# Optimization experiments

Measured on AMD Instinct MI355X. Metric: run time of the kernel, lower is better.

The kernel has to match this reference:

```python
import jax, jax.numpy as jnp
import numpy as np

Y_SCALE = 0.01  # fixed weight quantization scale (q_scale of the int8 weights)


def setup_inputs() -> dict:
    key = jax.random.key(0)
    kx, kw, kb = jax.random.split(key, 3)
    B, S, IN, OUT = 4, 2048, 4096, 4096
    x = jax.random.normal(kx, (B, S, IN), dtype=jnp.float32)
    # int8 quantized weights, stored transposed as (in_features, out_features)
    weight_q = jax.random.randint(kw, (IN, OUT), -128, 128, dtype=jnp.int32)
    bias = jax.random.normal(kb, (OUT,), dtype=jnp.float32)
    return {"x": x, "weight_q": weight_q, "bias": bias}


def reference(x, weight_q, bias):
    # Per-batch-sample dynamic activation scale: max(|x_i|)/128 over each [S, IN] slice
    x_scale = jnp.max(jnp.abs(x), axis=(1, 2), keepdims=True) / 128.0  # [B,1,1]
    # int8 quantize: round + clip
    xq = jnp.clip(jnp.round(x / x_scale), -128, 127).astype(jnp.int8)  # [B,S,IN]
    wq = weight_q.astype(jnp.int8)                                      # [IN,OUT]
    c = jax.lax.dot_general(
        xq, wq,
        dimension_numbers=(((2,), (0,)), ((), ())),
        preferred_element_type=jnp.int32,
    )  # [B,S,OUT]
    # dequantize and bias-add
    y = c.astype(jnp.float32) * (x_scale * Y_SCALE)
    return y + bias
```

## Files before the change

### kernel.cpp

```cpp
#include <hip/hip_runtime.h>
#include <stdint.h>

#define K_DIM 4096
#define N_DIM 4096
#define M_DIM 8192
#define S_ROWS 2048
#define NT 32

typedef int v4i __attribute__((ext_vector_type(4)));

__device__ __forceinline__ void gload16(const void* g, void* l) {
    __builtin_amdgcn_global_load_lds(
        (const __attribute__((address_space(1))) unsigned int*)g,
        (__attribute__((address_space(3))) unsigned int*)l, 16, 0, 0);
}

__device__ __forceinline__ void barrier() {
    asm volatile("" ::: "memory");
    __builtin_amdgcn_s_barrier();
    asm volatile("" ::: "memory");
}

__global__ void prep1_kernel(const float* __restrict__ x, unsigned* __restrict__ amax,
                             const int* __restrict__ wq, char* __restrict__ wt) {
    __shared__ unsigned lds[64 * 17];
    if (blockIdx.x < 4096) {
        int b = blockIdx.x >> 10;
        int bx = blockIdx.x & 1023;
        const float4* xb = (const float4*)(x + (size_t)b * S_ROWS * K_DIM);
        int tid = bx * 256 + threadIdx.x;
        const int stride = 1024 * 256;
        float m = 0.f;
#pragma unroll
        for (int i = 0; i < 8; ++i) {
            float4 v = xb[tid + i * stride];
            m = fmaxf(m, fmaxf(fmaxf(fabsf(v.x), fabsf(v.y)),
                               fmaxf(fabsf(v.z), fabsf(v.w))));
        }
#pragma unroll
        for (int off = 32; off; off >>= 1)
            m = fmaxf(m, __shfl_xor(m, off));
        float* red = (float*)lds;
        if ((threadIdx.x & 63) == 0) red[threadIdx.x >> 6] = m;
        __syncthreads();
        if (threadIdx.x == 0) {
            m = fmaxf(fmaxf(red[0], red[1]), fmaxf(red[2], red[3]));
            atomicMax(&amax[b], __float_as_uint(m));
        }
    } else {
        int wb = blockIdx.x - 4096;
        int n0 = (wb & 63) * 64;
        int k0 = (wb >> 6) * 64;
        int t = threadIdx.x;
        int c = t & 63;
        int g = t >> 6;
#pragma unroll
        for (int rep = 0; rep < 4; ++rep) {
            int kb = g * 16 + rep * 4;
            int v0 = wq[(size_t)(k0 + kb + 0) * N_DIM + n0 + c];
            int v1 = wq[(size_t)(k0 + kb + 1) * N_DIM + n0 + c];
            int v2 = wq[(size_t)(k0 + kb + 2) * N_DIM + n0 + c];
            int v3 = wq[(size_t)(k0 + kb + 3) * N_DIM + n0 + c];
            lds[c * 17 + (kb >> 2)] =
                (v0 & 255) | ((v1 & 255) << 8) | ((v2 & 255) << 16) | ((v3 & 255) << 24);
        }
        __syncthreads();
        int row = t >> 2;
        int ch = t & 3;
        uint4 o;
        o.x = lds[row * 17 + ch * 4 + 0];
        o.y = lds[row * 17 + ch * 4 + 1];
        o.z = lds[row * 17 + ch * 4 + 2];
        o.w = lds[row * 17 + ch * 4 + 3];
        *(uint4*)(wt + (size_t)(n0 + row) * K_DIM + k0 + ch * 16) = o;
    }
}

__global__ void quant_kernel(const float* __restrict__ x,
                             const unsigned* __restrict__ amax,
                             char* __restrict__ xq) {
    size_t gid = (size_t)blockIdx.x * 256 + threadIdx.x;
    size_t base = gid * 16;
    int b = (int)(base >> 23);
    float inv = 128.0f / __uint_as_float(amax[b]);
    const float4* xs = (const float4*)(x + base);
    unsigned parts[4];
#pragma unroll
    for (int i = 0; i < 4; ++i) {
        float4 v = xs[i];
        int q0 = max(-128, min(127, (int)rintf(v.x * inv)));
        int q1 = max(-128, min(127, (int)rintf(v.y * inv)));
        int q2 = max(-128, min(127, (int)rintf(v.z * inv)));
        int q3 = max(-128, min(127, (int)rintf(v.w * inv)));
        parts[i] = (q0 & 255) | ((q1 & 255) << 8) | ((q2 & 255) << 16) | ((q3 & 255) << 24);
    }
    *(uint4*)(xq + base) = make_uint4(parts[0], parts[1], parts[2], parts[3]);
}

__global__ __launch_bounds__(512, 2) void gemm8_kernel(
    const char* __restrict__ A, const char* __restrict__ Bt,
    const float* __restrict__ bias, const unsigned* __restrict__ amax,
    float* __restrict__ out) {
    __shared__ char sm[131072];
    const int t = threadIdx.x;
    const int l = t & 63;
    const int w = t >> 6;
    const int wm = w >> 2;
    const int wn = w & 3;
    const int rb = l & 15;
    const int sg = l >> 4;

    int bid = blockIdx.x;
    int swz = (bid & 7) * 64 + (bid >> 3);
    int mt = swz >> 4, nt = swz & 15;
    const size_t m0 = (size_t)mt * 256;
    const size_t n0 = (size_t)nt * 256;

    const int s0 = (sg ^ (rb & 7)) << 4;
    const int s1 = s0 ^ 64;
    const int baseA = (wm * 128 + rb) * 128;
    const int baseB = 32768 + (wn * 64 + rb) * 128;

    v4i acc[8][4];
#pragma unroll
    for (int i = 0; i < 8; ++i)
#pragma unroll
        for (int j = 0; j < 4; ++j) acc[i][j] = (v4i){0, 0, 0, 0};

#define ST_FULL(tt)                                                          \
    if ((tt) < NT) {                                                         \
        char* lb = sm + (((tt) & 1) << 16);                                  \
        const char* ga = A + m0 * K_DIM + (size_t)(tt) * 128;                \
        const char* gb = Bt + n0 * K_DIM + (size_t)(tt) * 128;               \
        _Pragma("unroll")                                                    \
        for (int j = 0; j < 4; ++j) {                                        \
            int p = j * 512 + t;                                             \
            int r = p >> 3, sl = p & 7;                                      \
            int s = sl ^ (r & 7);                                            \
            gload16(ga + (size_t)r * K_DIM + s * 16, lb + p * 16);           \
        }                                                                    \
        _Pragma("unroll")                                                    \
        for (int j = 0; j < 4; ++j) {                                        \
            int p = j * 512 + t;                                             \
            int r = p >> 3, sl = p & 7;                                      \
            int s = sl ^ (r & 7);                                            \
            gload16(gb + (size_t)r * K_DIM + s * 16, lb + 32768 + p * 16);   \
        }                                                                    \
    }

    ST_FULL(0);

    v4i aF[4][2], aG[4][2], bF[4][2];

    for (int i = 0; i < NT; ++i) {
        const char* pb = sm + ((i & 1) << 16);
        const char* pA0 = pb + baseA + s0;
        const char* pA1 = pb + baseA + s1;
        const char* pB0 = pb + baseB + s0;
        const char* pB1 = pb + baseB + s1;

        asm volatile("s_waitcnt vmcnt(0)" ::: "memory");
        barrier();

#pragma unroll
        for (int mi = 0; mi < 4; ++mi) {
            aF[mi][0] = *(const v4i*)(pA0 + mi * 2048);
            aF[mi][1] = *(const v4i*)(pA1 + mi * 2048);
        }
#pragma unroll
        for (int ni = 0; ni < 4; ++ni) {
            bF[ni][0] = *(const v4i*)(pB0 + ni * 2048);
            bF[ni][1] = *(const v4i*)(pB1 + ni * 2048);
        }
#pragma unroll
        for (int mi = 0; mi < 4; ++mi) {
            aG[mi][0] = *(const v4i*)(pA0 + mi * 2048 + 8192);
            aG[mi][1] = *(const v4i*)(pA1 + mi * 2048 + 8192);
        }

        ST_FULL(i + 1);

        __builtin_amdgcn_s_setprio(1);
#pragma unroll
        for (int mi = 0; mi < 4; ++mi)
#pragma unroll
            for (int ni = 0; ni < 4; ++ni)
#pragma unroll
                for (int ks = 0; ks < 2; ++ks)
                    acc[mi][ni] = __builtin_amdgcn_mfma_i32_16x16x64_i8(
                        aF[mi][ks], bF[ni][ks], acc[mi][ni], 0, 0, 0);
#pragma unroll
        for (int mi = 0; mi < 4; ++mi)
#pragma unroll
            for (int ni = 0; ni < 4; ++ni)
#pragma unroll
                for (int ks = 0; ks < 2; ++ks)
                    acc[mi + 4][ni] = __builtin_amdgcn_mfma_i32_16x16x64_i8(
                        aG[mi][ks], bF[ni][ks], acc[mi + 4][ni], 0, 0, 0);
        __builtin_amdgcn_s_setprio(0);
    }

    float scale = __uint_as_float(amax[m0 >> 11]) * (1.0f / 128.0f) * 0.01f;
    float bv[4];
#pragma unroll
    for (int ni = 0; ni < 4; ++ni) bv[ni] = bias[n0 + wn * 64 + ni * 16 + rb];
#pragma unroll
    for (int mi = 0; mi < 8; ++mi) {
#pragma unroll
        for (int rg = 0; rg < 4; ++rg) {
            size_t row = m0 + wm * 128 + mi * 16 + sg * 4 + rg;
            float* orow = out + row * N_DIM + n0 + wn * 64 + rb;
#pragma unroll
            for (int ni = 0; ni < 4; ++ni)
                orow[ni * 16] = (float)acc[mi][ni][rg] * scale + bv[ni];
        }
    }
#undef ST_FULL
}

extern "C" void kernel_launch(void* const* d_in, const int* in_sizes, int n_in,
                              void* d_out, int out_size, void* d_ws, size_t ws_size,
                              hipStream_t stream) {
    const float* x = (const float*)d_in[0];
    const int* wq = (const int*)d_in[1];
    const float* bias = (const float*)d_in[2];
    float* out = (float*)d_out;

    unsigned* amax = (unsigned*)d_ws;
    char* xq = (char*)d_ws + 256;
    char* wt = (char*)d_ws + 256 + (size_t)M_DIM * K_DIM;

    hipMemsetAsync(d_ws, 0, 16, stream);

    prep1_kernel<<<dim3(8192), 256, 0, stream>>>(x, amax, wq, wt);
    quant_kernel<<<8192, 256, 0, stream>>>(x, amax, xq);
    gemm8_kernel<<<dim3(512), 512, 0, stream>>>(xq, wt, bias, amax, out);
}
```

Before: 218.5 us.

## Load A fragments directly from global memory into registers, keep only B in LDS

The GEMM no longer stages the activation tile A through shared memory. Each warp now loads its A fragments straight from global memory into registers and prefetches the next k-tile between the two MFMA halves. Only B is double-buffered in LDS, which halves shared memory use and could allow two blocks per CU. In exchange, A is re-read by each of the four column warps instead of being shared, which raises global/L2 traffic and the exposed load latency.

```diff
diff --git a/kernel.cpp b/kernel.cpp
--- a/kernel.cpp
+++ b/kernel.cpp
@@ -101,7 +101,7 @@
     const char* __restrict__ A, const char* __restrict__ Bt,
     const float* __restrict__ bias, const unsigned* __restrict__ amax,
     float* __restrict__ out) {
-    __shared__ char sm[131072];
+    __shared__ char sm[65536];
     const int t = threadIdx.x;
     const int l = t & 63;
     const int w = t >> 6;
@@ -118,8 +118,9 @@
 
     const int s0 = (sg ^ (rb & 7)) << 4;
     const int s1 = s0 ^ 64;
-    const int baseA = (wm * 128 + rb) * 128;
-    const int baseB = 32768 + (wn * 64 + rb) * 128;
+    const int baseB = (wn * 64 + rb) * 128;
+
+    const char* aBase = A + (m0 + wm * 128 + rb) * (size_t)K_DIM + sg * 16;
 
     v4i acc[8][4];
 #pragma unroll
@@ -127,58 +128,48 @@
 #pragma unroll
         for (int j = 0; j < 4; ++j) acc[i][j] = (v4i){0, 0, 0, 0};
 
-#define ST_FULL(tt)                                                          \
+#define ST_B(tt)                                                             \
     if ((tt) < NT) {                                                         \
-        char* lb = sm + (((tt) & 1) << 16);                                  \
-        const char* ga = A + m0 * K_DIM + (size_t)(tt) * 128;                \
+        char* lb = sm + (((tt) & 1) << 15);                                  \
         const char* gb = Bt + n0 * K_DIM + (size_t)(tt) * 128;               \
         _Pragma("unroll")                                                    \
         for (int j = 0; j < 4; ++j) {                                        \
             int p = j * 512 + t;                                             \
             int r = p >> 3, sl = p & 7;                                      \
             int s = sl ^ (r & 7);                                            \
-            gload16(ga + (size_t)r * K_DIM + s * 16, lb + p * 16);           \
+            gload16(gb + (size_t)r * K_DIM + s * 16, lb + p * 16);           \
         }                                                                    \
-        _Pragma("unroll")                                                    \
-        for (int j = 0; j < 4; ++j) {                                        \
-            int p = j * 512 + t;                                             \
-            int r = p >> 3, sl = p & 7;                                      \
-            int s = sl ^ (r & 7);                                            \
-            gload16(gb + (size_t)r * K_DIM + s * 16, lb + 32768 + p * 16);   \
-        }                                                                    \
-    }
-
-    ST_FULL(0);
+    }
+
+#define LD_A(dst, mrow, tt, ks)                                              \
+    dst = *(const v4i*)(aBase + (size_t)(mrow) * (16 * K_DIM) +              \
+                        (size_t)(tt) * 128 + (ks) * 64);
 
     v4i aF[4][2], aG[4][2], bF[4][2];
 
+    ST_B(0);
+#pragma unroll
+    for (int mi = 0; mi < 4; ++mi) {
+        LD_A(aF[mi][0], mi, 0, 0); LD_A(aF[mi][1], mi, 0, 1);
+        LD_A(aG[mi][0], mi + 4, 0, 0); LD_A(aG[mi][1], mi + 4, 0, 1);
+    }
+
     for (int i = 0; i < NT; ++i) {
-        const char* pb = sm + ((i & 1) << 16);
-        const char* pA0 = pb + baseA + s0;
-        const char* pA1 = pb + baseA + s1;
+        const char* pb = sm + ((i & 1) << 15);
         const char* pB0 = pb + baseB + s0;
         const char* pB1 = pb + baseB + s1;
+        const int nx = (i + 1 < NT) ? (i + 1) : (NT - 1);
 
         asm volatile("s_waitcnt vmcnt(0)" ::: "memory");
         barrier();
 
-#pragma unroll
-        for (int mi = 0; mi < 4; ++mi) {
-            aF[mi][0] = *(const v4i*)(pA0 + mi * 2048);
-            aF[mi][1] = *(const v4i*)(pA1 + mi * 2048);
-        }
+        ST_B(i + 1);
+
 #pragma unroll
         for (int ni = 0; ni < 4; ++ni) {
             bF[ni][0] = *(const v4i*)(pB0 + ni * 2048);
             bF[ni][1] = *(const v4i*)(pB1 + ni * 2048);
         }
-#pragma unroll
-        for (int mi = 0; mi < 4; ++mi) {
-            aG[mi][0] = *(const v4i*)(pA0 + mi * 2048 + 8192);
-            aG[mi][1] = *(const v4i*)(pA1 + mi * 2048 + 8192);
-        }
-
-        ST_FULL(i + 1);
 
         __builtin_amdgcn_s_setprio(1);
 #pragma unroll
@@ -189,6 +180,14 @@
                 for (int ks = 0; ks < 2; ++ks)
                     acc[mi][ni] = __builtin_amdgcn_mfma_i32_16x16x64_i8(
                         aF[mi][ks], bF[ni][ks], acc[mi][ni], 0, 0, 0);
+        __builtin_amdgcn_s_setprio(0);
+
+#pragma unroll
+        for (int mi = 0; mi < 4; ++mi) {
+            LD_A(aF[mi][0], mi, nx, 0); LD_A(aF[mi][1], mi, nx, 1);
+        }
+
+        __builtin_amdgcn_s_setprio(1);
 #pragma unroll
         for (int mi = 0; mi < 4; ++mi)
 #pragma unroll
@@ -198,6 +197,11 @@
                     acc[mi + 4][ni] = __builtin_amdgcn_mfma_i32_16x16x64_i8(
                         aG[mi][ks], bF[ni][ks], acc[mi + 4][ni], 0, 0, 0);
         __builtin_amdgcn_s_setprio(0);
+
+#pragma unroll
+        for (int mi = 0; mi < 4; ++mi) {
+            LD_A(aG[mi][0], mi + 4, nx, 0); LD_A(aG[mi][1], mi + 4, nx, 1);
+        }
     }
 
     float scale = __uint_as_float(amax[m0 >> 11]) * (1.0f / 128.0f) * 0.01f;
@@ -215,7 +219,8 @@
                 orow[ni * 16] = (float)acc[mi][ni][rg] * scale + bv[ni];
         }
     }
-#undef ST_FULL
+#undef ST_B
+#undef LD_A
 }
 
 extern "C" void kernel_launch(void* const* d_in, const int* in_sizes, int n_in,
```

After: 406.0 us. +85.9%, slower.

## Issue next-tile LDS loads earlier and stream A fragments between MFMA groups

Applied to the files above, without the earlier changes.

The int8 GEMM main loop now issues the global-to-LDS loads for the next tile right after a barrier. It then waits with a partial vmcnt so only the current tile's loads must have landed. A-operand fragments are no longer all preloaded (16 v4i registers). They are read from LDS in pairs interleaved with the MFMA groups, which cuts register pressure and lets LDS reads overlap matrix math. In exchange there is an extra barrier per iteration, and the MFMAs may stall on fresh LDS reads if the compiler does not schedule them ahead.

```diff
diff --git a/kernel.cpp b/kernel.cpp
--- a/kernel.cpp
+++ b/kernel.cpp
@@ -148,9 +148,17 @@
         }                                                                    \
     }
 
+#define MFMA_PAIR(accrow, afrag)                                             \
+    _Pragma("unroll")                                                        \
+    for (int ni = 0; ni < 4; ++ni)                                           \
+        _Pragma("unroll")                                                    \
+        for (int ks = 0; ks < 2; ++ks)                                       \
+            acc[accrow][ni] = __builtin_amdgcn_mfma_i32_16x16x64_i8(         \
+                afrag[ks], bF[ni][ks], acc[accrow][ni], 0, 0, 0);
+
     ST_FULL(0);
 
-    v4i aF[4][2], aG[4][2], bF[4][2];
+    v4i aP[2][2], bF[4][2];
 
     for (int i = 0; i < NT; ++i) {
         const char* pb = sm + ((i & 1) << 16);
@@ -159,44 +167,30 @@
         const char* pB0 = pb + baseB + s0;
         const char* pB1 = pb + baseB + s1;
 
-        asm volatile("s_waitcnt vmcnt(0)" ::: "memory");
         barrier();
-
-#pragma unroll
-        for (int mi = 0; mi < 4; ++mi) {
-            aF[mi][0] = *(const v4i*)(pA0 + mi * 2048);
-            aF[mi][1] = *(const v4i*)(pA1 + mi * 2048);
-        }
+        ST_FULL(i + 1);
+        if (i == NT - 1) { asm volatile("s_waitcnt vmcnt(0)" ::: "memory"); }
+        else             { asm volatile("s_waitcnt vmcnt(8)" ::: "memory"); }
+        barrier();
+
 #pragma unroll
         for (int ni = 0; ni < 4; ++ni) {
             bF[ni][0] = *(const v4i*)(pB0 + ni * 2048);
             bF[ni][1] = *(const v4i*)(pB1 + ni * 2048);
         }
-#pragma unroll
-        for (int mi = 0; mi < 4; ++mi) {
-            aG[mi][0] = *(const v4i*)(pA0 + mi * 2048 + 8192);
-            aG[mi][1] = *(const v4i*)(pA1 + mi * 2048 + 8192);
-        }
-
-        ST_FULL(i + 1);
-
+        aP[0][0] = *(const v4i*)(pA0 + 0 * 2048); aP[0][1] = *(const v4i*)(pA1 + 0 * 2048);
+        aP[1][0] = *(const v4i*)(pA0 + 1 * 2048); aP[1][1] = *(const v4i*)(pA1 + 1 * 2048);
         __builtin_amdgcn_s_setprio(1);
-#pragma unroll
-        for (int mi = 0; mi < 4; ++mi)
-#pragma unroll
-            for (int ni = 0; ni < 4; ++ni)
-#pragma unroll
-                for (int ks = 0; ks < 2; ++ks)
-                    acc[mi][ni] = __builtin_amdgcn_mfma_i32_16x16x64_i8(
-                        aF[mi][ks], bF[ni][ks], acc[mi][ni], 0, 0, 0);
-#pragma unroll
-        for (int mi = 0; mi < 4; ++mi)
-#pragma unroll
-            for (int ni = 0; ni < 4; ++ni)
-#pragma unroll
-                for (int ks = 0; ks < 2; ++ks)
-                    acc[mi + 4][ni] = __builtin_amdgcn_mfma_i32_16x16x64_i8(
-                        aG[mi][ks], bF[ni][ks], acc[mi + 4][ni], 0, 0, 0);
+        MFMA_PAIR(0, aP[0]); MFMA_PAIR(1, aP[1]);
+        aP[0][0] = *(const v4i*)(pA0 + 2 * 2048); aP[0][1] = *(const v4i*)(pA1 + 2 * 2048);
+        aP[1][0] = *(const v4i*)(pA0 + 3 * 2048); aP[1][1] = *(const v4i*)(pA1 + 3 * 2048);
+        MFMA_PAIR(2, aP[0]); MFMA_PAIR(3, aP[1]);
+        aP[0][0] = *(const v4i*)(pA0 + 0 * 2048 + 8192); aP[0][1] = *(const v4i*)(pA1 + 0 * 2048 + 8192);
+        aP[1][0] = *(const v4i*)(pA0 + 1 * 2048 + 8192); aP[1][1] = *(const v4i*)(pA1 + 1 * 2048 + 8192);
+        MFMA_PAIR(4, aP[0]); MFMA_PAIR(5, aP[1]);
+        aP[0][0] = *(const v4i*)(pA0 + 2 * 2048 + 8192); aP[0][1] = *(const v4i*)(pA1 + 2 * 2048 + 8192);
+        aP[1][0] = *(const v4i*)(pA0 + 3 * 2048 + 8192); aP[1][1] = *(const v4i*)(pA1 + 3 * 2048 + 8192);
+        MFMA_PAIR(6, aP[0]); MFMA_PAIR(7, aP[1]);
         __builtin_amdgcn_s_setprio(0);
     }
 
@@ -216,6 +210,7 @@
         }
     }
 #undef ST_FULL
+#undef MFMA_PAIR
 }
 
 extern "C" void kernel_launch(void* const* d_in, const int* in_sizes, int n_in,
```

After: 225.2 us. 1.03x slower.

## Shrink GEMM tile to 256x128 with triple-buffered K=64 pipeline

Applied to the files above, without the earlier changes.

Reworks the int8 GEMM to use 256x128 output tiles, a K step of 64, and a three-stage LDS ring buffer that keeps two loads in flight, waiting on vmcnt(3) instead of draining each iteration. LDS per block falls to 72KB and launch bounds rise to allow more blocks per CU, with twice as many blocks and a new XCD-aware tile mapping. The aim is better latency hiding and occupancy. The cost is lower arithmetic intensity per tile, so more global and LDS traffic per MFMA, and more barriers per unit of work.

```diff
diff --git a/kernel.cpp b/kernel.cpp
--- a/kernel.cpp
+++ b/kernel.cpp
@@ -5,7 +5,7 @@
 #define N_DIM 4096
 #define M_DIM 8192
 #define S_ROWS 2048
-#define NT 32
+#define NKT 64
 
 typedef int v4i __attribute__((ext_vector_type(4)));
 
@@ -97,107 +97,93 @@
     *(uint4*)(xq + base) = make_uint4(parts[0], parts[1], parts[2], parts[3]);
 }
 
-__global__ __launch_bounds__(512, 2) void gemm8_kernel(
+__global__ __launch_bounds__(512, 4) void gemm8_kernel(
     const char* __restrict__ A, const char* __restrict__ Bt,
     const float* __restrict__ bias, const unsigned* __restrict__ amax,
     float* __restrict__ out) {
-    __shared__ char sm[131072];
+    __shared__ char sm[73728];
     const int t = threadIdx.x;
     const int l = t & 63;
     const int w = t >> 6;
-    const int wm = w >> 2;
-    const int wn = w & 3;
+    const int wm = w >> 1;
+    const int wn = w & 1;
     const int rb = l & 15;
     const int sg = l >> 4;
 
     int bid = blockIdx.x;
-    int swz = (bid & 7) * 64 + (bid >> 3);
-    int mt = swz >> 4, nt = swz & 15;
+    int xcd = bid & 7;
+    int idx = bid >> 3;
+    int mt = (xcd << 2) | (idx >> 5);
+    int nt = idx & 31;
     const size_t m0 = (size_t)mt * 256;
-    const size_t n0 = (size_t)nt * 256;
-
-    const int s0 = (sg ^ (rb & 7)) << 4;
-    const int s1 = s0 ^ 64;
-    const int baseA = (wm * 128 + rb) * 128;
-    const int baseB = 32768 + (wn * 64 + rb) * 128;
-
-    v4i acc[8][4];
-#pragma unroll
-    for (int i = 0; i < 8; ++i)
+    const size_t n0 = (size_t)nt * 128;
+
+    const int lineA = wm * 32 + (rb >> 1);
+    const int lineB = wn * 32 + (rb >> 1);
+    const int svBase = ((rb & 1) << 2) | sg;
+    const int offA = lineA * 128 + ((svBase ^ (lineA & 7)) << 4);
+    const int offB = 16384 + lineB * 128 + ((svBase ^ (lineB & 7)) << 4);
+
+    v4i acc[4][4];
+#pragma unroll
+    for (int i = 0; i < 4; ++i)
 #pragma unroll
         for (int j = 0; j < 4; ++j) acc[i][j] = (v4i){0, 0, 0, 0};
 
-#define ST_FULL(tt)                                                          \
-    if ((tt) < NT) {                                                         \
-        char* lb = sm + (((tt) & 1) << 16);                                  \
-        const char* ga = A + m0 * K_DIM + (size_t)(tt) * 128;                \
-        const char* gb = Bt + n0 * K_DIM + (size_t)(tt) * 128;               \
+#define ST_FULL(tt, bsel)                                                    \
+    if ((tt) < NKT) {                                                        \
+        char* lb = sm + (bsel) * 24576;                                      \
+        const char* ga = A + m0 * K_DIM + (size_t)(tt) * 64;                 \
+        const char* gb = Bt + n0 * K_DIM + (size_t)(tt) * 64;                \
         _Pragma("unroll")                                                    \
-        for (int j = 0; j < 4; ++j) {                                        \
+        for (int j = 0; j < 2; ++j) {                                        \
             int p = j * 512 + t;                                             \
-            int r = p >> 3, sl = p & 7;                                      \
-            int s = sl ^ (r & 7);                                            \
-            gload16(ga + (size_t)r * K_DIM + s * 16, lb + p * 16);           \
+            int line = p >> 3, sl = p & 7;                                   \
+            int sv = sl ^ (line & 7);                                        \
+            int r = line * 2 + (sv >> 2), ks = sv & 3;                       \
+            gload16(ga + (size_t)r * K_DIM + ks * 16, lb + p * 16);          \
         }                                                                    \
-        _Pragma("unroll")                                                    \
-        for (int j = 0; j < 4; ++j) {                                        \
-            int p = j * 512 + t;                                             \
-            int r = p >> 3, sl = p & 7;                                      \
-            int s = sl ^ (r & 7);                                            \
-            gload16(gb + (size_t)r * K_DIM + s * 16, lb + 32768 + p * 16);   \
+        {                                                                    \
+            int p = t;                                                       \
+            int line = p >> 3, sl = p & 7;                                   \
+            int sv = sl ^ (line & 7);                                        \
+            int r = line * 2 + (sv >> 2), ks = sv & 3;                       \
+            gload16(gb + (size_t)r * K_DIM + ks * 16, lb + 16384 + p * 16);  \
         }                                                                    \
     }
 
-    ST_FULL(0);
-
-    v4i aF[4][2], aG[4][2], bF[4][2];
-
-    for (int i = 0; i < NT; ++i) {
-        const char* pb = sm + ((i & 1) << 16);
-        const char* pA0 = pb + baseA + s0;
-        const char* pA1 = pb + baseA + s1;
-        const char* pB0 = pb + baseB + s0;
-        const char* pB1 = pb + baseB + s1;
-
-        asm volatile("s_waitcnt vmcnt(0)" ::: "memory");
+    ST_FULL(0, 0);
+    ST_FULL(1, 1);
+
+    v4i aF[4], bF[4];
+    int cur = 0;
+
+    for (int i = 0; i < NKT; ++i) {
+        if (i == NKT - 1) { asm volatile("s_waitcnt vmcnt(0)" ::: "memory"); }
+        else             { asm volatile("s_waitcnt vmcnt(3)" ::: "memory"); }
         barrier();
 
-#pragma unroll
-        for (int mi = 0; mi < 4; ++mi) {
-            aF[mi][0] = *(const v4i*)(pA0 + mi * 2048);
-            aF[mi][1] = *(const v4i*)(pA1 + mi * 2048);
-        }
-#pragma unroll
-        for (int ni = 0; ni < 4; ++ni) {
-            bF[ni][0] = *(const v4i*)(pB0 + ni * 2048);
-            bF[ni][1] = *(const v4i*)(pB1 + ni * 2048);
-        }
-#pragma unroll
-        for (int mi = 0; mi < 4; ++mi) {
-            aG[mi][0] = *(const v4i*)(pA0 + mi * 2048 + 8192);
-            aG[mi][1] = *(const v4i*)(pA1 + mi * 2048 + 8192);
-        }
-
-        ST_FULL(i + 1);
+        int s2 = cur + 2; if (s2 >= 3) s2 -= 3;
+        ST_FULL(i + 2, s2);
+
+        const char* pb = sm + cur * 24576;
+        const char* pA = pb + offA;
+        const char* pB = pb + offB;
+#pragma unroll
+        for (int ni = 0; ni < 4; ++ni) bF[ni] = *(const v4i*)(pB + ni * 1024);
+#pragma unroll
+        for (int mi = 0; mi < 4; ++mi) aF[mi] = *(const v4i*)(pA + mi * 1024);
 
         __builtin_amdgcn_s_setprio(1);
 #pragma unroll
         for (int mi = 0; mi < 4; ++mi)
 #pragma unroll
             for (int ni = 0; ni < 4; ++ni)
-#pragma unroll
-                for (int ks = 0; ks < 2; ++ks)
-                    acc[mi][ni] = __builtin_amdgcn_mfma_i32_16x16x64_i8(
-                        aF[mi][ks], bF[ni][ks], acc[mi][ni], 0, 0, 0);
-#pragma unroll
-        for (int mi = 0; mi < 4; ++mi)
-#pragma unroll
-            for (int ni = 0; ni < 4; ++ni)
-#pragma unroll
-                for (int ks = 0; ks < 2; ++ks)
-                    acc[mi + 4][ni] = __builtin_amdgcn_mfma_i32_16x16x64_i8(
-                        aG[mi][ks], bF[ni][ks], acc[mi + 4][ni], 0, 0, 0);
+                acc[mi][ni] = __builtin_amdgcn_mfma_i32_16x16x64_i8(
+                    aF[mi], bF[ni], acc[mi][ni], 0, 0, 0);
         __builtin_amdgcn_s_setprio(0);
+
+        cur = (cur == 2) ? 0 : cur + 1;
     }
 
     float scale = __uint_as_float(amax[m0 >> 11]) * (1.0f / 128.0f) * 0.01f;
@@ -205,10 +191,10 @@
 #pragma unroll
     for (int ni = 0; ni < 4; ++ni) bv[ni] = bias[n0 + wn * 64 + ni * 16 + rb];
 #pragma unroll
-    for (int mi = 0; mi < 8; ++mi) {
+    for (int mi = 0; mi < 4; ++mi) {
 #pragma unroll
         for (int rg = 0; rg < 4; ++rg) {
-            size_t row = m0 + wm * 128 + mi * 16 + sg * 4 + rg;
+            size_t row = m0 + wm * 64 + mi * 16 + sg * 4 + rg;
             float* orow = out + row * N_DIM + n0 + wn * 64 + rb;
 #pragma unroll
             for (int ni = 0; ni < 4; ++ni)
@@ -234,5 +220,5 @@
 
     prep1_kernel<<<dim3(8192), 256, 0, stream>>>(x, amax, wq, wt);
     quant_kernel<<<8192, 256, 0, stream>>>(x, amax, xq);
-    gemm8_kernel<<<dim3(512), 512, 0, stream>>>(xq, wt, bias, amax, out);
-}
+    gemm8_kernel<<<dim3(1024), 512, 0, stream>>>(xq, wt, bias, amax, out);
+}
```

Result: slower. 241.5 us (+10.6%).
